# Kernel tuning notes

Hardware: AMD Instinct MI355X
Metric: run time of the kernel (lower is better)

The kernel has to match this reference:

```python
import jax, jax.numpy as jnp
import numpy as np

NUM_ENTITIES = 100000
NUM_TIMES = 10000
D = 512
DB = 768
NUM_REL = 200
NUM_BASES = 4
N_NODES = 30000
N_EDGES = 200000
B = 128
P_ENT = 64
P_TIME = 32
T_UNIQ = 2000


def setup_inputs() -> dict:
    key = jax.random.key(0)
    ks = jax.random.split(key, 32)
    n = jax.random.normal
    ri = jax.random.randint
    inp = {}
    # learned params
    inp['emb'] = n(ks[0], (NUM_ENTITIES + NUM_TIMES, D), jnp.float32) * 0.05
    sc = 1.0 / np.sqrt(D)
    inp['basis1'] = n(ks[1], (NUM_BASES, D, D), jnp.float32) * sc
    inp['att1'] = n(ks[2], (NUM_REL, NUM_BASES), jnp.float32) * 0.5
    inp['root1'] = n(ks[3], (D, D), jnp.float32) * sc
    inp['bias1'] = jnp.zeros((D,), jnp.float32)
    inp['basis2'] = n(ks[4], (NUM_BASES, D, D), jnp.float32) * sc
    inp['att2'] = n(ks[5], (NUM_REL, NUM_BASES), jnp.float32) * 0.5
    inp['root2'] = n(ks[6], (D, D), jnp.float32) * sc
    inp['bias2'] = jnp.zeros((D,), jnp.float32)
    sb = 1.0 / np.sqrt(DB)
    inp['W_lin'] = n(ks[7], (DB, D), jnp.float32) * sb
    inp['b_lin'] = jnp.zeros((D,), jnp.float32)
    inp['W_attn'] = n(ks[8], (DB, D), jnp.float32) * sb
    inp['b_attn'] = jnp.zeros((D,), jnp.float32)
    inp['W_prob'] = n(ks[9], (DB, 1), jnp.float32) * sb
    inp['b_prob'] = jnp.zeros((1,), jnp.float32)
    # forward tensor args
    inp['ques_emb_bert'] = n(ks[10], (B, DB), jnp.float32)
    inp['x_idx'] = ri(ks[11], (N_NODES,), 0, NUM_ENTITIES, jnp.int32)
    inp['edge_index'] = ri(ks[12], (2, N_EDGES), 0, N_NODES, jnp.int32)
    inp['edge_type'] = ri(ks[13], (N_EDGES,), 0, NUM_REL, jnp.int32)
    inp['start_time'] = ri(ks[14], (N_EDGES,), 0, NUM_TIMES, jnp.int32)
    inp['end_time'] = ri(ks[15], (N_EDGES,), 0, NUM_TIMES, jnp.int32)
    inp['edge_batch_idx'] = jnp.sort(ri(ks[16], (N_EDGES,), 0, B, jnp.int32))
    inp['edge_norm'] = jax.random.uniform(ks[17], (N_EDGES,), jnp.float32)
    inp['uniq_times'] = ri(ks[18], (T_UNIQ,), 0, NUM_TIMES, jnp.int32)
    # padded index vectors: positions >= count point at the appended zero row
    ent_counts = ri(ks[19], (B,), 1, P_ENT + 1, jnp.int32)
    time_counts = ri(ks[20], (B,), 1, P_TIME + 1, jnp.int32)
    pe = ri(ks[21], (B, P_ENT), 0, N_NODES, jnp.int32)
    pt = ri(ks[22], (B, P_TIME), 0, T_UNIQ, jnp.int32)
    inp['padded_ent'] = jnp.where(jnp.arange(P_ENT)[None, :] < ent_counts[:, None], pe, N_NODES)
    inp['padded_time'] = jnp.where(jnp.arange(P_TIME)[None, :] < time_counts[:, None], pt, T_UNIQ)
    inp['ent_counts'] = ent_counts
    inp['time_counts'] = time_counts
    return inp


def rgcn_layer(x, basis, att, root, bias, src, dst, etype, st_emb, et_emb, q_t, edge_norm):
    # basis decomposition: project all nodes through each basis once. [N, NB, D]
    xb = jnp.einsum('ni,bio->nbo', x, basis)
    coeff = att[etype]                                 # [E, NB]
    msg = jnp.einsum('eb,ebd->ed', coeff, xb[src])     # [E, D]
    # time gate: question-time embedding vs edge interval midpoint embedding
    gate = jax.nn.sigmoid(jnp.sum(q_t * 0.5 * (st_emb + et_emb), axis=-1))  # [E]
    msg = msg * (gate * edge_norm)[:, None]
    agg = jax.ops.segment_sum(msg, dst, num_segments=N_NODES)
    return agg + x @ root + bias


def reference(emb, basis1, att1, root1, bias1, basis2, att2, root2, bias2,
              W_lin, b_lin, W_attn, b_attn, W_prob, b_prob,
              ques_emb_bert, x_idx, edge_index, edge_type, start_time, end_time,
              edge_batch_idx, edge_norm, uniq_times, padded_ent, padded_time,
              ent_counts, time_counts):
    question_embedding = ques_emb_bert @ W_lin + b_lin                  # [B, D]
    time_for_edge_attn = (ques_emb_bert @ W_attn + b_attn)[edge_batch_idx]  # [E, D]
    st_emb = emb[start_time + NUM_ENTITIES]
    et_emb = emb[end_time + NUM_ENTITIES]
    x = emb[x_idx]                                                      # [N, D]
    src, dst = edge_index[0], edge_index[1]
    h = jax.nn.relu(rgcn_layer(x, basis1, att1, root1, bias1, src, dst, edge_type,
                               st_emb, et_emb, time_for_edge_attn, edge_norm))
    # dropout is identity in eval mode
    h = rgcn_layer(h, basis2, att2, root2, bias2, src, dst, edge_type,
                   st_emb, et_emb, time_for_edge_attn, edge_norm)       # [N, D]
    subgraph_time_emb = emb[uniq_times + NUM_ENTITIES]                  # [T_u, D]
    zero = jnp.zeros((1, D), h.dtype)
    ent_w_zeros = jnp.concatenate([h, zero], axis=0)
    time_w_zeros = jnp.concatenate([subgraph_time_emb, zero], axis=0)
    pooled_ent = jnp.sum(ent_w_zeros[padded_ent], axis=1) / ent_counts[:, None].astype(h.dtype)
    pooled_time = jnp.sum(time_w_zeros[padded_time], axis=1) / time_counts[:, None].astype(h.dtype)
    p_ent = jax.nn.sigmoid(ques_emb_bert @ W_prob + b_prob)             # [B, 1]
    pred = (question_embedding + pooled_ent * p_ent + pooled_time * (1.0 - p_ent)) / 3.0
    # batched cosine similarity against full entity+time vocab
    pred_n = pred / jnp.maximum(jnp.linalg.norm(pred, axis=-1, keepdims=True), 1e-8)
    emb_n = emb / jnp.maximum(jnp.linalg.norm(emb, axis=-1, keepdims=True), 1e-8)
    score = pred_n @ emb_n.T                                            # [B, V]
    return score * 30.0
```

## Files before the change

### kernel.cpp

```cpp
#include <hip/hip_runtime.h>

#define NUM_ENT   100000
#define NTIMES    10000
#define DD        512
#define DB        768
#define NREL      200
#define NBAS      4
#define NN        30000
#define NEDGE     200000
#define BATCH     128
#define PENT      64
#define PTIME     32
#define TUNIQ     2000
#define V_TOT     110000
#define V_PAD     110208
#define VT16      6888
#define M_PAD2    30208
#define MT2R      1888
#define KT_L      80
#define KT_E      16

typedef __attribute__((ext_vector_type(8))) short s8v;
typedef __attribute__((ext_vector_type(4))) float f4v;

__device__ __forceinline__ unsigned short f2bf(float x){
  unsigned int u = __builtin_bit_cast(unsigned int, x);
  u += 0x7fffu + ((u >> 16) & 1u);
  return (unsigned short)(u >> 16);
}
__device__ __forceinline__ float bf2f(unsigned short h){
  unsigned int u = ((unsigned int)h) << 16;
  return __builtin_bit_cast(float, u);
}

__device__ __forceinline__ void gload16(const void* g, void* l){
  __builtin_amdgcn_global_load_lds(
      (const __attribute__((address_space(1))) void*)g,
      (__attribute__((address_space(3))) void*)l, 16, 0, 0);
}


__global__ __launch_bounds__(256) void k_conv_emb(const float* __restrict__ emb,
    unsigned short* __restrict__ Bp, float* __restrict__ invn){
  int vt = blockIdx.x;
  int wid = threadIdx.x >> 6, lane = threadIdx.x & 63;
  int vrow = vt * 16 + (lane & 15);
  float ss = 0.f;
  __shared__ float ssw[4][16];
  for (int i = 0; i < 4; ++i){
    int kt = wid + i * 4;
    int k0 = kt * 32 + (lane >> 4) * 8;
    s8v o;
    if (vrow < V_TOT){
      const float4* p = reinterpret_cast<const float4*>(emb + (size_t)vrow * DD + k0);
      float4 v0 = p[0], v1 = p[1];
      ss += v0.x*v0.x + v0.y*v0.y + v0.z*v0.z + v0.w*v0.w;
      ss += v1.x*v1.x + v1.y*v1.y + v1.z*v1.z + v1.w*v1.w;
      o[0] = (short)f2bf(v0.x); o[1] = (short)f2bf(v0.y);
      o[2] = (short)f2bf(v0.z); o[3] = (short)f2bf(v0.w);
      o[4] = (short)f2bf(v1.x); o[5] = (short)f2bf(v1.y);
      o[6] = (short)f2bf(v1.z); o[7] = (short)f2bf(v1.w);
    } else {
      #pragma unroll
      for (int j = 0; j < 8; ++j) o[j] = 0;
    }
    *reinterpret_cast<s8v*>(Bp + ((size_t)(kt * VT16 + vt) << 9) + lane * 8) = o;
  }
  ss += __shfl_xor(ss, 16);
  ss += __shfl_xor(ss, 32);
  if ((lane >> 4) == 0) ssw[wid][lane] = ss;
  __syncthreads();
  if (threadIdx.x < 16){
    float s = ssw[0][threadIdx.x] + ssw[1][threadIdx.x] + ssw[2][threadIdx.x] + ssw[3][threadIdx.x];
    int v = vt * 16 + threadIdx.x;
    invn[v] = (v < V_TOT) ? (1.0f / fmaxf(sqrtf(s), 1e-8f)) : 0.0f;
  }
}

__global__ __launch_bounds__(256) void k_small2(const float* __restrict__ ques,
    const float* __restrict__ Wl, const float* __restrict__ bl,
    const float* __restrict__ Wa, const float* __restrict__ ba,
    const float* __restrict__ Wp, const float* __restrict__ bp,
    float* __restrict__ qlin, float* __restrict__ qattn, float* __restrict__ pent){
  if (blockIdx.x == 32){
    int b = threadIdx.x >> 1, half = threadIdx.x & 1;
    float a = 0.f;
    int k0 = half * 384;
    for (int k = k0; k < k0 + 384; ++k)
      a = fmaf(ques[(size_t)b * DB + k], Wp[k], a);
    a += __shfl_xor(a, 1);
    if (half == 0) pent[b] = 1.f / (1.f + expf(-(a + bp[0])));
    return;
  }
  __shared__ float sq[128 * 96];
  int col = threadIdx.x & 31, bg = threadIdx.x >> 5;
  int c0 = blockIdx.x * 32;
  const float* W = (c0 < 512) ? Wl : Wa;
  int wcol = (c0 & 511) + col;
  float acc[16] = {};
  for (int k0 = 0; k0 < DB; k0 += 96){
    __syncthreads();
    for (int i = threadIdx.x; i < 128 * 96; i += 256){
      int b = i / 96, kk = i - b * 96;
      sq[i] = ques[(size_t)b * DB + k0 + kk];
    }
    __syncthreads();
    for (int kk = 0; kk < 96; kk += 4){
      float w0 = W[(size_t)(k0 + kk + 0) * 512 + wcol];
      float w1 = W[(size_t)(k0 + kk + 1) * 512 + wcol];
      float w2 = W[(size_t)(k0 + kk + 2) * 512 + wcol];
      float w3 = W[(size_t)(k0 + kk + 3) * 512 + wcol];
      #pragma unroll
      for (int bb = 0; bb < 16; ++bb){
        float4 qv = *reinterpret_cast<const float4*>(&sq[(bg * 16 + bb) * 96 + kk]);
        acc[bb] = fmaf(qv.x, w0, fmaf(qv.y, w1, fmaf(qv.z, w2, fmaf(qv.w, w3, acc[bb]))));
      }
    }
  }
  float* dst = (c0 < 512) ? qlin : qattn;
  const float* bias = (c0 < 512) ? bl : ba;
  #pragma unroll
  for (int bb = 0; bb < 16; ++bb)
    dst[(size_t)(bg * 16 + bb) * 512 + wcol] = acc[bb] + bias[wcol];
}

__global__ __launch_bounds__(256) void k_pack_qrows(const float* __restrict__ src,
    unsigned short* __restrict__ Ap){
  int w = (int)((blockIdx.x * 256 + threadIdx.x) >> 6);
  int lane = threadIdx.x & 63;
  if (w >= BATCH) return;
  const float* p = src + (size_t)w * 512 + lane * 8;
  s8v o;
  #pragma unroll
  for (int j = 0; j < 8; ++j) o[j] = (short)f2bf(p[j]);
  *reinterpret_cast<s8v*>(Ap + ((size_t)((w >> 4) * KT_E + (lane >> 2)) << 9)
                             + ((w & 15) + (lane & 3) * 16) * 8) = o;
}

__global__ __launch_bounds__(256) void k_pack_B(const float* __restrict__ basis,
    const float* __restrict__ root, unsigned short* __restrict__ Bp){
  int idx = blockIdx.x * 256 + threadIdx.x;
  if (idx >= KT_L * 32 * 64) return;
  int lane = idx & 63; int kt = idx >> 11;
  int k0 = kt * 32 + (lane >> 4) * 8;
  int col = ((idx >> 6) & 31) * 16 + (lane & 15);
  s8v o;
  #pragma unroll
  for (int j = 0; j < 8; ++j){
    int k = k0 + j;
    float v = (k < 2048) ? basis[(size_t)k * 512 + col] : root[(size_t)(k - 2048) * 512 + col];
    o[j] = (short)f2bf(v);
  }
  *reinterpret_cast<s8v*>(Bp + (size_t)idx * 8) = o;
}

template<int MODE>
__global__ __launch_bounds__(512, 2) void k_gemm256(
    const unsigned short* __restrict__ A, const unsigned short* __restrict__ B,
    const float* __restrict__ bias, unsigned short* __restrict__ outh){
  __shared__ __align__(1024) short sAll[3 * 16384];
  const int Kt = KT_L;
  int tid = threadIdx.x;
  int lane = tid & 63, wid = tid >> 6;
  int wr = wid >> 2, wc = wid & 3;
  const int q = 29, r = 4;
  int g = blockIdx.x;
  int xcd = g & 7, i = g >> 3;
  int ng = (xcd < r ? xcd * (q + 1) : r * (q + 1) + (xcd - r) * q) + i;
  int blkM = ng >> 1, blkN = ng & 1;
  int rt0 = blkM * 16;
  int ct0 = blkN * 16;
  const unsigned short* pA0 = A + ((size_t)(rt0 + wid) * Kt) * 512 + lane * 8;
  const unsigned short* pA1 = A + ((size_t)(rt0 + 8 + wid) * Kt) * 512 + lane * 8;
  const unsigned short* pB0 = B + (size_t)(ct0 + wid) * 512 + lane * 8;
  const unsigned short* pB1 = B + (size_t)(ct0 + 8 + wid) * 512 + lane * 8;
  const size_t gbs = 32 * 512;
  int soA0 = wid * 512, soA1 = (8 + wid) * 512;
  f4v acc[8][4] = {};

  auto STAGE = [&](int buf, int kt){
    short* b = &sAll[buf * 16384];
    gload16(pA0 + (size_t)kt * 512, b + soA0);
    gload16(pA1 + (size_t)kt * 512, b + soA1);
    gload16(pB0 + (size_t)kt * gbs, b + 8192 + soA0);
    gload16(pB1 + (size_t)kt * gbs, b + 8192 + soA1);
  };
  auto COMPUTE = [&](int buf){
    const short* base = &sAll[buf * 16384];
    s8v af[8], bfr[4];
    #pragma unroll
    for (int m = 0; m < 8; ++m) af[m] = *reinterpret_cast<const s8v*>(base + (wr * 8 + m) * 512 + lane * 8);
    #pragma unroll
    for (int n = 0; n < 4; ++n) bfr[n] = *reinterpret_cast<const s8v*>(base + 8192 + (wc * 4 + n) * 512 + lane * 8);
    __builtin_amdgcn_s_setprio(1);
    #pragma unroll
    for (int m = 0; m < 8; ++m)
      #pragma unroll
      for (int n = 0; n < 4; ++n)
        acc[m][n] = __builtin_amdgcn_mfma_f32_16x16x32_bf16(af[m], bfr[n], acc[m][n], 0, 0, 0);
    __builtin_amdgcn_s_setprio(0);
  };

  STAGE(0, 0);
  STAGE(1, 1);
  int cb = 0, sb = 2;
  for (int kt = 0; kt < Kt - 2; ++kt){
    STAGE(sb, kt + 2);
    asm volatile("s_waitcnt vmcnt(8)" ::: "memory");
    __builtin_amdgcn_s_barrier();
    __builtin_amdgcn_sched_barrier(0);
    COMPUTE(cb);
    __builtin_amdgcn_s_barrier();
    cb = (cb == 2) ? 0 : cb + 1;
    sb = (sb == 2) ? 0 : sb + 1;
  }
  asm volatile("s_waitcnt vmcnt(4)" ::: "memory");
  __builtin_amdgcn_s_barrier();
  __builtin_amdgcn_sched_barrier(0);
  COMPUTE(cb);
  cb = (cb == 2) ? 0 : cb + 1;
  asm volatile("s_waitcnt vmcnt(0)" ::: "memory");
  __builtin_amdgcn_s_barrier();
  __builtin_amdgcn_sched_barrier(0);
  COMPUTE(cb);

  int R0 = blkM * 256 + wr * 128 + (lane >> 4) * 4;
  int C0 = blkN * 256 + wc * 64 + (lane & 15);
  #pragma unroll
  for (int m = 0; m < 8; ++m)
    #pragma unroll
    for (int n = 0; n < 4; ++n){
      int col = C0 + n * 16;
      float bb = bias[col];
      #pragma unroll
      for (int rr4 = 0; rr4 < 4; ++rr4){
        int rr = R0 + m * 16 + rr4;
        if (rr < NN){
          float v = acc[m][n][rr4] + bb;
          if constexpr (MODE == 1) v = fmaxf(v, 0.f);
          outh[(size_t)rr * 512 + col] = f2bf(v);
        }
      }
    }
}

template<int MODE>
__global__ __launch_bounds__(256) void k_gemm(
    const unsigned short* __restrict__ A, const unsigned short* __restrict__ B,
    int Kt, int Bt_stride, int ct_off,
    const float* __restrict__ invn, float* __restrict__ outf){
  __shared__ __align__(1024) short sAll[3 * 8192];
  int tid = threadIdx.x;
  int lane = tid & 63, wid = tid >> 6;
  int wr = wid >> 1, wc = wid & 1;
  int rt0 = blockIdx.x * 8;
  int ct0 = blockIdx.y * 8;
  int ctB = ct0 + ct_off;
  const unsigned short* pA0 = A + ((size_t)(rt0 + 2 * wid) * Kt) * 512 + lane * 8;
  const unsigned short* pA1 = pA0 + (size_t)Kt * 512;
  const unsigned short* pB0 = B + (size_t)(ctB + 2 * wid) * 512 + lane * 8;
  const unsigned short* pB1 = pB0 + 512;
  size_t gbs = (size_t)Bt_stride * 512;
  int so = 2 * wid * 512;
  f4v acc[4][4] = {};

  auto STAGE = [&](int buf, int kt){
    short* b = &sAll[buf * 8192];
    gload16(pA0 + (size_t)kt * 512, b + so);
    gload16(pA1 + (size_t)kt * 512, b + so + 512);
    gload16(pB0 + (size_t)kt * gbs, b + 4096 + so);
    gload16(pB1 + (size_t)kt * gbs, b + 4096 + so + 512);
  };
  auto COMPUTE = [&](int buf){
    const short* base = &sAll[buf * 8192];
    s8v af[4], bfr[4];
    #pragma unroll
    for (int m = 0; m < 4; ++m) af[m] = *reinterpret_cast<const s8v*>(base + (wr * 4 + m) * 512 + lane * 8);
    #pragma unroll
    for (int n = 0; n < 4; ++n) bfr[n] = *reinterpret_cast<const s8v*>(base + 4096 + (wc * 4 + n) * 512 + lane * 8);
    #pragma unroll
    for (int m = 0; m < 4; ++m)
      #pragma unroll
      for (int n = 0; n < 4; ++n)
        acc[m][n] = __builtin_amdgcn_mfma_f32_16x16x32_bf16(af[m], bfr[n], acc[m][n], 0, 0, 0);
  };

  STAGE(0, 0);
  STAGE(1, 1);
  int cb = 0, sb = 2;
  for (int kt = 0; kt < Kt - 2; ++kt){
    STAGE(sb, kt + 2);
    asm volatile("s_waitcnt vmcnt(8)" ::: "memory");
    __builtin_amdgcn_s_barrier();
    __builtin_amdgcn_sched_barrier(0);
    COMPUTE(cb);
    __builtin_amdgcn_s_barrier();
    cb = (cb == 2) ? 0 : cb + 1;
    sb = (sb == 2) ? 0 : sb + 1;
  }
  asm volatile("s_waitcnt vmcnt(4)" ::: "memory");
  __builtin_amdgcn_s_barrier();
  __builtin_amdgcn_sched_barrier(0);
  COMPUTE(cb);
  cb = (cb == 2) ? 0 : cb + 1;
  asm volatile("s_waitcnt vmcnt(0)" ::: "memory");
  __builtin_amdgcn_s_barrier();
  __builtin_amdgcn_sched_barrier(0);
  COMPUTE(cb);

  #pragma unroll
  for (int m = 0; m < 4; ++m)
    #pragma unroll
    for (int n = 0; n < 4; ++n){
      int row0 = rt0 * 16 + (wr * 4 + m) * 16 + ((lane >> 4) * 4);
      int col  = (ct0 + wc * 4 + n) * 16 + (lane & 15);
      #pragma unroll
      for (int r = 0; r < 4; ++r){
        float c = acc[m][n][r];
        int rr = row0 + r;
        if constexpr (MODE == 0){
          if (col < NTIMES) outf[(size_t)rr * NTIMES + col] = c;
        } else {
          if (col < V_TOT) outf[(size_t)rr * V_TOT + col] = c * invn[col] * 30.0f;
        }
      }
    }
}

__global__ __launch_bounds__(256) void k_edge_w(const int* __restrict__ ebatch,
    const int* __restrict__ st, const int* __restrict__ et,
    const float* __restrict__ enorm, const float* __restrict__ M2,
    float* __restrict__ we){
  int e = blockIdx.x * 256 + threadIdx.x;
  if (e >= NEDGE) return;
  int b = ebatch[e];
  float s = 0.5f * (M2[(size_t)b * NTIMES + st[e]] + M2[(size_t)b * NTIMES + et[e]]);
  we[e] = (1.f / (1.f + expf(-s))) * enorm[e];
}

__global__ __launch_bounds__(256) void k_count(const int* __restrict__ ei,
    int* __restrict__ cnt, int* __restrict__ lists){
  int e = blockIdx.x * 256 + threadIdx.x;
  if (e >= NEDGE) return;
  int dst = ei[NEDGE + e];
  int slot = atomicAdd(&cnt[dst], 1);
  if (slot < 64) lists[(size_t)dst * 64 + slot] = e;
}

__global__ __launch_bounds__(256) void k_gather_x(const int* __restrict__ x_idx,
    const unsigned short* __restrict__ Bp, unsigned short* __restrict__ Ap,
    unsigned short* __restrict__ x_rm){
  int w = (int)((blockIdx.x * 256 + threadIdx.x) >> 6);
  int lane = threadIdx.x & 63;
  if (w >= NN) return;
  int v = x_idx[w];
  s8v x = *reinterpret_cast<const s8v*>(
      Bp + ((size_t)(lane >> 2) * VT16 + (v >> 4)) * 512 + ((v & 15) + (lane & 3) * 16) * 8);
  *reinterpret_cast<s8v*>(x_rm + (size_t)w * 512 + lane * 8) = x;
  *reinterpret_cast<s8v*>(Ap + ((size_t)(w >> 4) * KT_L + 64 + (lane >> 2)) * 512
                             + ((w & 15) + (lane & 3) * 16) * 8) = x;
}

__global__ __launch_bounds__(256) void k_pack_rows(const unsigned short* __restrict__ src_rm,
    unsigned short* __restrict__ Ap){
  int w = (int)((blockIdx.x * 256 + threadIdx.x) >> 6);
  int lane = threadIdx.x & 63;
  if (w >= NN) return;
  s8v x = *reinterpret_cast<const s8v*>(src_rm + (size_t)w * 512 + lane * 8);
  *reinterpret_cast<s8v*>(Ap + ((size_t)(w >> 4) * KT_L + 64 + (lane >> 2)) * 512
                             + ((w & 15) + (lane & 3) * 16) * 8) = x;
}

__global__ __launch_bounds__(256) void k_edge_agg(const unsigned short* __restrict__ xsrc,
    const int* __restrict__ ei, const int* __restrict__ etype,
    const float* __restrict__ we, const float* __restrict__ att,
    const int* __restrict__ cnt, const int* __restrict__ lists,
    unsigned short* __restrict__ Ap){
  __shared__ float satt[NREL * NBAS];
  __shared__ int sed[4][64];
  for (int i = threadIdx.x; i < NREL * NBAS; i += 256) satt[i] = att[i];
  int wid = threadIdx.x >> 6, lane = threadIdx.x & 63;
  int n = blockIdx.x * 4 + wid;
  int deg = min(cnt[n], 64);
  int eid = (lane < deg) ? lists[(size_t)n * 64 + lane] : 0x7fffffff;
  int rank = 0;
  for (int j = 0; j < 64; ++j){
    int v = __shfl(eid, j);
    rank += (v < eid) ? 1 : 0;
  }
  __syncthreads();
  if (lane < deg) sed[wid][rank] = eid;
  __syncthreads();
  float acc[NBAS][8] = {};
  if (deg > 0){
    int my_e = sed[wid][(lane < deg) ? lane : 0];
    int my_s = ei[my_e];
    int my_t = etype[my_e];
    float my_w = we[my_e];
    float c0l = my_w * satt[my_t * 4 + 0];
    float c1l = my_w * satt[my_t * 4 + 1];
    float c2l = my_w * satt[my_t * 4 + 2];
    float c3l = my_w * satt[my_t * 4 + 3];
    int s0 = __shfl(my_s, 0);
    s8v xv = *reinterpret_cast<const s8v*>(xsrc + (size_t)s0 * 512 + lane * 8);
    for (int j = 0; j < deg; ++j){
      s8v xn = xv;
      if (j + 1 < deg){
        int sn = __shfl(my_s, j + 1);
        xn = *reinterpret_cast<const s8v*>(xsrc + (size_t)sn * 512 + lane * 8);
      }
      float c0 = __shfl(c0l, j), c1 = __shfl(c1l, j);
      float c2 = __shfl(c2l, j), c3 = __shfl(c3l, j);
      #pragma unroll
      for (int jj = 0; jj < 8; ++jj){
        float x = bf2f((unsigned short)xv[jj]);
        acc[0][jj] = fmaf(c0, x, acc[0][jj]);
        acc[1][jj] = fmaf(c1, x, acc[1][jj]);
        acc[2][jj] = fmaf(c2, x, acc[2][jj]);
        acc[3][jj] = fmaf(c3, x, acc[3][jj]);
      }
      xv = xn;
    }
  }
  #pragma unroll
  for (int b = 0; b < NBAS; ++b){
    s8v o;
    #pragma unroll
    for (int jj = 0; jj < 8; ++jj) o[jj] = (short)f2bf(acc[b][jj]);
    *reinterpret_cast<s8v*>(Ap + ((size_t)(n >> 4) * KT_L + b * 16 + (lane >> 2)) * 512
                               + ((n & 15) + (lane & 3) * 16) * 8) = o;
  }
}

__global__ __launch_bounds__(256) void k_pred(const unsigned short* __restrict__ h2,
    const float* __restrict__ emb, const int* __restrict__ uniq,
    const int* __restrict__ pent_idx, const int* __restrict__ ptime_idx,
    const int* __restrict__ ent_c, const int* __restrict__ time_c,
    const float* __restrict__ qlin, const float* __restrict__ pent,
    unsigned short* __restrict__ Ap_pred){
  int w = (int)((blockIdx.x * 256 + threadIdx.x) >> 6);
  int lane = threadIdx.x & 63;
  if (w >= BATCH) return;
  float ae[8] = {}, at[8] = {};
  for (int j = 0; j < PENT; ++j){
    int idx = pent_idx[w * PENT + j];
    if (idx < NN){
      s8v hv = *reinterpret_cast<const s8v*>(h2 + (size_t)idx * 512 + lane * 8);
      #pragma unroll
      for (int jj = 0; jj < 8; ++jj) ae[jj] += bf2f((unsigned short)hv[jj]);
    }
  }
  for (int j = 0; j < PTIME; ++j){
    int ti = ptime_idx[w * PTIME + j];
    if (ti < TUNIQ){
      const float* p = emb + (size_t)(NUM_ENT + uniq[ti]) * 512 + lane * 8;
      #pragma unroll
      for (int jj = 0; jj < 8; ++jj) at[jj] += p[jj];
    }
  }
  float ce = 1.f / (float)ent_c[w], ct = 1.f / (float)time_c[w];
  float p = pent[w];
  float pr[8]; float ss = 0.f;
  #pragma unroll
  for (int jj = 0; jj < 8; ++jj){
    float v = (qlin[(size_t)w * 512 + lane * 8 + jj] + ae[jj] * ce * p + at[jj] * ct * (1.f - p)) * (1.f / 3.f);
    pr[jj] = v; ss += v * v;
  }
  ss += __shfl_xor(ss, 32); ss += __shfl_xor(ss, 16); ss += __shfl_xor(ss, 8);
  ss += __shfl_xor(ss, 4);  ss += __shfl_xor(ss, 2);  ss += __shfl_xor(ss, 1);
  float inv = 1.f / fmaxf(sqrtf(ss), 1e-8f);
  s8v o;
  #pragma unroll
  for (int jj = 0; jj < 8; ++jj) o[jj] = (short)f2bf(pr[jj] * inv);
  *reinterpret_cast<s8v*>(Ap_pred + ((size_t)((w >> 4) * KT_E + (lane >> 2)) << 9)
                                  + ((w & 15) + (lane & 3) * 16) * 8) = o;
}

extern "C" void kernel_launch(void* const* d_in, const int* in_sizes, int n_in,
                              void* d_out, int out_size, void* d_ws, size_t ws_size,
                              hipStream_t stream){
  const float* emb    = (const float*)d_in[0];
  const float* basis1 = (const float*)d_in[1];
  const float* att1   = (const float*)d_in[2];
  const float* root1  = (const float*)d_in[3];
  const float* bias1  = (const float*)d_in[4];
  const float* basis2 = (const float*)d_in[5];
  const float* att2   = (const float*)d_in[6];
  const float* root2  = (const float*)d_in[7];
  const float* bias2  = (const float*)d_in[8];
  const float* W_lin  = (const float*)d_in[9];
  const float* b_lin  = (const float*)d_in[10];
  const float* W_attn = (const float*)d_in[11];
  const float* b_attn = (const float*)d_in[12];
  const float* W_prob = (const float*)d_in[13];
  const float* b_prob = (const float*)d_in[14];
  const float* ques   = (const float*)d_in[15];
  const int* x_idx    = (const int*)d_in[16];
  const int* eidx     = (const int*)d_in[17];
  const int* etype    = (const int*)d_in[18];
  const int* stime    = (const int*)d_in[19];
  const int* etime    = (const int*)d_in[20];
  const int* ebatch   = (const int*)d_in[21];
  const float* enorm  = (const float*)d_in[22];
  const int* uniq     = (const int*)d_in[23];
  const int* pent_i   = (const int*)d_in[24];
  const int* ptime_i  = (const int*)d_in[25];
  const int* ent_c    = (const int*)d_in[26];
  const int* time_c   = (const int*)d_in[27];
  float* out = (float*)d_out;

  char* w = (char*)d_ws;
  size_t off = 0;
  auto alloc = [&](size_t bytes)->char*{ char* p = w + off; off += (bytes + 255) & ~(size_t)255; return p; };
  unsigned short* Bp_emb = (unsigned short*)alloc((size_t)KT_E * VT16 * 1024);
  float*          invn   = (float*)alloc((size_t)V_PAD * 4);
  unsigned short* Ap     = (unsigned short*)alloc((size_t)MT2R * KT_L * 1024);
  unsigned short* B1p    = (unsigned short*)alloc((size_t)KT_L * 32 * 1024);
  unsigned short* B2p    = (unsigned short*)alloc((size_t)KT_L * 32 * 1024);
  char* xh_base = alloc((size_t)NN * 512 * 2 * 2);
  unsigned short* x_rm = (unsigned short*)xh_base;
  unsigned short* h1   = (unsigned short*)(xh_base + (size_t)NN * 512 * 2);
  unsigned short* h2   = (unsigned short*)xh_base;
  float* M2    = (float*)alloc((size_t)BATCH * NTIMES * 4);
  float* we    = (float*)alloc((size_t)NEDGE * 4);
  float* qlin  = (float*)alloc((size_t)BATCH * 512 * 4);
  float* qattn = (float*)alloc((size_t)BATCH * 512 * 4);
  float* pent  = (float*)alloc(1024);
  unsigned short* Apq    = (unsigned short*)alloc((size_t)8 * KT_E * 1024);
  unsigned short* Appred = (unsigned short*)alloc((size_t)8 * KT_E * 1024);
  int* cnt   = (int*)alloc((size_t)NN * 4);
  int* lists = (int*)alloc((size_t)NN * 64 * 4);
  (void)ws_size; (void)in_sizes; (void)n_in; (void)out_size;

  k_conv_emb<<<VT16, 256, 0, stream>>>(emb, Bp_emb, invn);
  k_small2<<<33, 256, 0, stream>>>(ques, W_lin, b_lin, W_attn, b_attn, W_prob, b_prob,
                                   qlin, qattn, pent);
  k_pack_qrows<<<32, 256, 0, stream>>>(qattn, Apq);
  k_pack_B<<<(KT_L * 32 * 64 + 255) / 256, 256, 0, stream>>>(basis1, root1, B1p);
  k_pack_B<<<(KT_L * 32 * 64 + 255) / 256, 256, 0, stream>>>(basis2, root2, B2p);
  k_gemm<0><<<dim3(1, 79), 256, 0, stream>>>(Apq, Bp_emb, KT_E, VT16, NUM_ENT / 16,
                                             nullptr, M2);
  k_edge_w<<<(NEDGE + 255) / 256, 256, 0, stream>>>(ebatch, stime, etime, enorm, M2, we);
  hipMemsetAsync(cnt, 0, (size_t)NN * 4, stream);
  k_count<<<(NEDGE + 255) / 256, 256, 0, stream>>>(eidx, cnt, lists);
  k_gather_x<<<NN / 4, 256, 0, stream>>>(x_idx, Bp_emb, Ap, x_rm);
  k_edge_agg<<<NN / 4, 256, 0, stream>>>(x_rm, eidx, etype, we, att1, cnt, lists, Ap);
  k_gemm256<1><<<236, 512, 0, stream>>>(Ap, B1p, bias1, h1);
  k_pack_rows<<<NN / 4, 256, 0, stream>>>(h1, Ap);
  k_edge_agg<<<NN / 4, 256, 0, stream>>>(h1, eidx, etype, we, att2, cnt, lists, Ap);
  k_gemm256<2><<<236, 512, 0, stream>>>(Ap, B2p, bias2, h2);
  k_pred<<<32, 256, 0, stream>>>(h2, emb, uniq, pent_i, ptime_i, ent_c, time_c,
                                 qlin, pent, Appred);
  k_gemm<3><<<dim3(1, V_PAD / 128), 256, 0, stream>>>(Appred, Bp_emb, KT_E, VT16, 0,
                                                      invn, out);
}
```

Before: 764.6 us.

## Fuse embedding conversion into score GEMM and retile RGCN GEMMs

Drops the full-vocabulary bf16 pre-conversion pass. The final score kernel now reads fp32 embeddings directly, converts them to bf16 in LDS and computes the column norms on the fly. Only the time-embedding slice is packed for the M2 GEMM, and gather_x converts rows straight from fp32. Edge weighting and destination counting are fused into one kernel, the RGCN GEMMs are retiled to 256x128 tiles with twice as many blocks, and k_pred spreads its work over one block per batch row. The score kernel's register-staged loads with synchronous barriers may hide latency less well than the previous async LDS pipeline.

```diff
diff --git a/kernel.cpp b/kernel.cpp
--- a/kernel.cpp
+++ b/kernel.cpp
@@ -13,12 +13,11 @@
 #define PTIME     32
 #define TUNIQ     2000
 #define V_TOT     110000
-#define V_PAD     110208
-#define VT16      6888
 #define M_PAD2    30208
 #define MT2R      1888
 #define KT_L      80
 #define KT_E      16
+#define TCT       632
 
 typedef __attribute__((ext_vector_type(8))) short s8v;
 typedef __attribute__((ext_vector_type(4))) float f4v;
@@ -39,43 +38,6 @@
       (__attribute__((address_space(3))) void*)l, 16, 0, 0);
 }
 
-
-__global__ __launch_bounds__(256) void k_conv_emb(const float* __restrict__ emb,
-    unsigned short* __restrict__ Bp, float* __restrict__ invn){
-  int vt = blockIdx.x;
-  int wid = threadIdx.x >> 6, lane = threadIdx.x & 63;
-  int vrow = vt * 16 + (lane & 15);
-  float ss = 0.f;
-  __shared__ float ssw[4][16];
-  for (int i = 0; i < 4; ++i){
-    int kt = wid + i * 4;
-    int k0 = kt * 32 + (lane >> 4) * 8;
-    s8v o;
-    if (vrow < V_TOT){
-      const float4* p = reinterpret_cast<const float4*>(emb + (size_t)vrow * DD + k0);
-      float4 v0 = p[0], v1 = p[1];
-      ss += v0.x*v0.x + v0.y*v0.y + v0.z*v0.z + v0.w*v0.w;
-      ss += v1.x*v1.x + v1.y*v1.y + v1.z*v1.z + v1.w*v1.w;
-      o[0] = (short)f2bf(v0.x); o[1] = (short)f2bf(v0.y);
-      o[2] = (short)f2bf(v0.z); o[3] = (short)f2bf(v0.w);
-      o[4] = (short)f2bf(v1.x); o[5] = (short)f2bf(v1.y);
-      o[6] = (short)f2bf(v1.z); o[7] = (short)f2bf(v1.w);
-    } else {
-      #pragma unroll
-      for (int j = 0; j < 8; ++j) o[j] = 0;
-    }
-    *reinterpret_cast<s8v*>(Bp + ((size_t)(kt * VT16 + vt) << 9) + lane * 8) = o;
-  }
-  ss += __shfl_xor(ss, 16);
-  ss += __shfl_xor(ss, 32);
-  if ((lane >> 4) == 0) ssw[wid][lane] = ss;
-  __syncthreads();
-  if (threadIdx.x < 16){
-    float s = ssw[0][threadIdx.x] + ssw[1][threadIdx.x] + ssw[2][threadIdx.x] + ssw[3][threadIdx.x];
-    int v = vt * 16 + threadIdx.x;
-    invn[v] = (v < V_TOT) ? (1.0f / fmaxf(sqrtf(s), 1e-8f)) : 0.0f;
-  }
-}
 
 __global__ __launch_bounds__(256) void k_small2(const float* __restrict__ ques,
     const float* __restrict__ Wl, const float* __restrict__ bl,
@@ -154,51 +116,64 @@
   *reinterpret_cast<s8v*>(Bp + (size_t)idx * 8) = o;
 }
 
-template<int MODE>
-__global__ __launch_bounds__(512, 2) void k_gemm256(
+__global__ __launch_bounds__(256) void k_pack_temb(const float* __restrict__ emb,
+    unsigned short* __restrict__ Bt){
+  int idx = blockIdx.x * 256 + threadIdx.x;
+  if (idx >= KT_E * TCT * 64) return;
+  int lane = idx & 63;
+  int ct = (idx >> 6) % TCT;
+  int kt = idx / (TCT * 64);
+  int c = ct * 16 + (lane & 15);
+  int k0 = kt * 32 + (lane >> 4) * 8;
+  s8v o;
+  if (c < NTIMES){
+    const float* p = emb + (size_t)(NUM_ENT + c) * 512 + k0;
+    #pragma unroll
+    for (int j = 0; j < 8; ++j) o[j] = (short)f2bf(p[j]);
+  } else {
+    #pragma unroll
+    for (int j = 0; j < 8; ++j) o[j] = 0;
+  }
+  *reinterpret_cast<s8v*>(Bt + (size_t)idx * 8) = o;
+}
+
+__global__ __launch_bounds__(256) void k_gemm_m2(
     const unsigned short* __restrict__ A, const unsigned short* __restrict__ B,
-    const float* __restrict__ bias, unsigned short* __restrict__ outh){
-  __shared__ __align__(1024) short sAll[3 * 16384];
-  const int Kt = KT_L;
+    float* __restrict__ outf){
+  __shared__ __align__(1024) short sAll[3 * 8192];
+  const int Kt = KT_E;
   int tid = threadIdx.x;
   int lane = tid & 63, wid = tid >> 6;
-  int wr = wid >> 2, wc = wid & 3;
-  const int q = 29, r = 4;
-  int g = blockIdx.x;
-  int xcd = g & 7, i = g >> 3;
-  int ng = (xcd < r ? xcd * (q + 1) : r * (q + 1) + (xcd - r) * q) + i;
-  int blkM = ng >> 1, blkN = ng & 1;
-  int rt0 = blkM * 16;
-  int ct0 = blkN * 16;
-  const unsigned short* pA0 = A + ((size_t)(rt0 + wid) * Kt) * 512 + lane * 8;
-  const unsigned short* pA1 = A + ((size_t)(rt0 + 8 + wid) * Kt) * 512 + lane * 8;
-  const unsigned short* pB0 = B + (size_t)(ct0 + wid) * 512 + lane * 8;
-  const unsigned short* pB1 = B + (size_t)(ct0 + 8 + wid) * 512 + lane * 8;
-  const size_t gbs = 32 * 512;
-  int soA0 = wid * 512, soA1 = (8 + wid) * 512;
-  f4v acc[8][4] = {};
+  int wr = wid >> 1, wc = wid & 1;
+  int rt0 = blockIdx.x * 8;
+  int ct0 = blockIdx.y * 8;
+  const unsigned short* pA0 = A + ((size_t)(rt0 + 2 * wid) * Kt) * 512 + lane * 8;
+  const unsigned short* pA1 = pA0 + (size_t)Kt * 512;
+  const unsigned short* pB0 = B + (size_t)(ct0 + 2 * wid) * 512 + lane * 8;
+  const unsigned short* pB1 = pB0 + 512;
+  size_t gbs = (size_t)TCT * 512;
+  int so = 2 * wid * 512;
+  f4v acc[4][4] = {};
 
   auto STAGE = [&](int buf, int kt){
-    short* b = &sAll[buf * 16384];
-    gload16(pA0 + (size_t)kt * 512, b + soA0);
-    gload16(pA1 + (size_t)kt * 512, b + soA1);
-    gload16(pB0 + (size_t)kt * gbs, b + 8192 + soA0);
-    gload16(pB1 + (size_t)kt * gbs, b + 8192 + soA1);
+    short* b = &sAll[buf * 8192];
+    gload16(pA0 + (size_t)kt * 512, b + so);
+    gload16(pA1 + (size_t)kt * 512, b + so + 512);
+    gload16(pB0 + (size_t)kt * gbs, b + 4096 + so);
+    gload16(pB1 + (size_t)kt * gbs, b + 4096 + so + 512);
   };
   auto COMPUTE = [&](int buf){
-    const short* base = &sAll[buf * 16384];
-    s8v af[8], bfr[4];
-    #pragma unroll
-    for (int m = 0; m < 8; ++m) af[m] = *reinterpret_cast<const s8v*>(base + (wr * 8 + m) * 512 + lane * 8);
-    #pragma unroll
-    for (int n = 0; n < 4; ++n) bfr[n] = *reinterpret_cast<const s8v*>(base + 8192 + (wc * 4 + n) * 512 + lane * 8);
-    __builtin_amdgcn_s_setprio(1);
-    #pragma unroll
-    for (int m = 0; m < 8; ++m)
+    const short* base = &sAll[buf * 8192];
+    s8v af[4], bfr[4];
+    #pragma unroll
+    for (int m = 0; m < 4; ++m) af[m] = *reinterpret_cast<const s8v*>(base + (wr * 4 + m) * 512 + lane * 8);
+    #pragma unroll
+    for (int n = 0; n < 4; ++n) bfr[n] = *reinterpret_cast<const s8v*>(base + 4096 + (wc * 4 + n) * 512 + lane * 8);
+    #pragma unroll
+    for (int m = 0; m < 4; ++m)
       #pragma unroll
       for (int n = 0; n < 4; ++n)
         acc[m][n] = __builtin_amdgcn_mfma_f32_16x16x32_bf16(af[m], bfr[n], acc[m][n], 0, 0, 0);
-    __builtin_amdgcn_s_setprio(0);
   };
 
   STAGE(0, 0);
@@ -224,65 +199,61 @@
   __builtin_amdgcn_sched_barrier(0);
   COMPUTE(cb);
 
-  int R0 = blkM * 256 + wr * 128 + (lane >> 4) * 4;
-  int C0 = blkN * 256 + wc * 64 + (lane & 15);
-  #pragma unroll
-  for (int m = 0; m < 8; ++m)
+  #pragma unroll
+  for (int m = 0; m < 4; ++m)
     #pragma unroll
     for (int n = 0; n < 4; ++n){
-      int col = C0 + n * 16;
-      float bb = bias[col];
-      #pragma unroll
-      for (int rr4 = 0; rr4 < 4; ++rr4){
-        int rr = R0 + m * 16 + rr4;
-        if (rr < NN){
-          float v = acc[m][n][rr4] + bb;
-          if constexpr (MODE == 1) v = fmaxf(v, 0.f);
-          outh[(size_t)rr * 512 + col] = f2bf(v);
-        }
+      int row0 = rt0 * 16 + (wr * 4 + m) * 16 + ((lane >> 4) * 4);
+      int col  = (ct0 + wc * 4 + n) * 16 + (lane & 15);
+      #pragma unroll
+      for (int r = 0; r < 4; ++r){
+        int rr = row0 + r;
+        if (col < NTIMES) outf[(size_t)rr * NTIMES + col] = acc[m][n][r];
       }
     }
 }
 
 template<int MODE>
-__global__ __launch_bounds__(256) void k_gemm(
+__global__ __launch_bounds__(512, 4) void k_gemm256(
     const unsigned short* __restrict__ A, const unsigned short* __restrict__ B,
-    int Kt, int Bt_stride, int ct_off,
-    const float* __restrict__ invn, float* __restrict__ outf){
-  __shared__ __align__(1024) short sAll[3 * 8192];
+    const float* __restrict__ bias, unsigned short* __restrict__ outh){
+  __shared__ __align__(1024) short sAll[3 * 12288];
+  const int Kt = KT_L;
   int tid = threadIdx.x;
   int lane = tid & 63, wid = tid >> 6;
   int wr = wid >> 1, wc = wid & 1;
-  int rt0 = blockIdx.x * 8;
-  int ct0 = blockIdx.y * 8;
-  int ctB = ct0 + ct_off;
-  const unsigned short* pA0 = A + ((size_t)(rt0 + 2 * wid) * Kt) * 512 + lane * 8;
-  const unsigned short* pA1 = pA0 + (size_t)Kt * 512;
-  const unsigned short* pB0 = B + (size_t)(ctB + 2 * wid) * 512 + lane * 8;
-  const unsigned short* pB1 = pB0 + 512;
-  size_t gbs = (size_t)Bt_stride * 512;
-  int so = 2 * wid * 512;
+  int g = blockIdx.x;
+  int ng = (g & 7) * 59 + (g >> 3);
+  int blkM = ng >> 2, blkN = ng & 3;
+  int rt0 = blkM * 16;
+  int ct0 = blkN * 8;
+  const unsigned short* pA0 = A + ((size_t)(rt0 + wid) * Kt) * 512 + lane * 8;
+  const unsigned short* pA1 = A + ((size_t)(rt0 + 8 + wid) * Kt) * 512 + lane * 8;
+  const unsigned short* pB0 = B + (size_t)(ct0 + wid) * 512 + lane * 8;
+  const size_t gbs = 32 * 512;
+  int soA0 = wid * 512, soA1 = (8 + wid) * 512, soB = 8192 + wid * 512;
   f4v acc[4][4] = {};
 
   auto STAGE = [&](int buf, int kt){
-    short* b = &sAll[buf * 8192];
-    gload16(pA0 + (size_t)kt * 512, b + so);
-    gload16(pA1 + (size_t)kt * 512, b + so + 512);
-    gload16(pB0 + (size_t)kt * gbs, b + 4096 + so);
-    gload16(pB1 + (size_t)kt * gbs, b + 4096 + so + 512);
+    short* b = &sAll[buf * 12288];
+    gload16(pA0 + (size_t)kt * 512, b + soA0);
+    gload16(pA1 + (size_t)kt * 512, b + soA1);
+    gload16(pB0 + (size_t)kt * gbs, b + soB);
   };
   auto COMPUTE = [&](int buf){
-    const short* base = &sAll[buf * 8192];
+    const short* base = &sAll[buf * 12288];
     s8v af[4], bfr[4];
     #pragma unroll
     for (int m = 0; m < 4; ++m) af[m] = *reinterpret_cast<const s8v*>(base + (wr * 4 + m) * 512 + lane * 8);
     #pragma unroll
-    for (int n = 0; n < 4; ++n) bfr[n] = *reinterpret_cast<const s8v*>(base + 4096 + (wc * 4 + n) * 512 + lane * 8);
+    for (int n = 0; n < 4; ++n) bfr[n] = *reinterpret_cast<const s8v*>(base + 8192 + (wc * 4 + n) * 512 + lane * 8);
+    __builtin_amdgcn_s_setprio(1);
     #pragma unroll
     for (int m = 0; m < 4; ++m)
       #pragma unroll
       for (int n = 0; n < 4; ++n)
         acc[m][n] = __builtin_amdgcn_mfma_f32_16x16x32_bf16(af[m], bfr[n], acc[m][n], 0, 0, 0);
+    __builtin_amdgcn_s_setprio(0);
   };
 
   STAGE(0, 0);
@@ -290,7 +261,7 @@
   int cb = 0, sb = 2;
   for (int kt = 0; kt < Kt - 2; ++kt){
     STAGE(sb, kt + 2);
-    asm volatile("s_waitcnt vmcnt(8)" ::: "memory");
+    asm volatile("s_waitcnt vmcnt(6)" ::: "memory");
     __builtin_amdgcn_s_barrier();
     __builtin_amdgcn_sched_barrier(0);
     COMPUTE(cb);
@@ -298,7 +269,7 @@
     cb = (cb == 2) ? 0 : cb + 1;
     sb = (sb == 2) ? 0 : sb + 1;
   }
-  asm volatile("s_waitcnt vmcnt(4)" ::: "memory");
+  asm volatile("s_waitcnt vmcnt(3)" ::: "memory");
   __builtin_amdgcn_s_barrier();
   __builtin_amdgcn_sched_barrier(0);
   COMPUTE(cb);
@@ -308,54 +279,53 @@
   __builtin_amdgcn_sched_barrier(0);
   COMPUTE(cb);
 
+  int R0 = blkM * 256 + wr * 64 + (lane >> 4) * 4;
+  int C0 = blkN * 128 + wc * 64 + (lane & 15);
   #pragma unroll
   for (int m = 0; m < 4; ++m)
     #pragma unroll
     for (int n = 0; n < 4; ++n){
-      int row0 = rt0 * 16 + (wr * 4 + m) * 16 + ((lane >> 4) * 4);
-      int col  = (ct0 + wc * 4 + n) * 16 + (lane & 15);
-      #pragma unroll
-      for (int r = 0; r < 4; ++r){
-        float c = acc[m][n][r];
-        int rr = row0 + r;
-        if constexpr (MODE == 0){
-          if (col < NTIMES) outf[(size_t)rr * NTIMES + col] = c;
-        } else {
-          if (col < V_TOT) outf[(size_t)rr * V_TOT + col] = c * invn[col] * 30.0f;
+      int col = C0 + n * 16;
+      float bb = bias[col];
+      #pragma unroll
+      for (int r4 = 0; r4 < 4; ++r4){
+        int rr = R0 + m * 16 + r4;
+        if (rr < NN){
+          float v = acc[m][n][r4] + bb;
+          if constexpr (MODE == 1) v = fmaxf(v, 0.f);
+          outh[(size_t)rr * 512 + col] = f2bf(v);
         }
       }
     }
 }
 
-__global__ __launch_bounds__(256) void k_edge_w(const int* __restrict__ ebatch,
+__global__ __launch_bounds__(256) void k_edgeprep(const int* __restrict__ ebatch,
     const int* __restrict__ st, const int* __restrict__ et,
     const float* __restrict__ enorm, const float* __restrict__ M2,
-    float* __restrict__ we){
+    const int* __restrict__ ei,
+    float* __restrict__ we, int* __restrict__ cnt, int* __restrict__ lists){
   int e = blockIdx.x * 256 + threadIdx.x;
   if (e >= NEDGE) return;
   int b = ebatch[e];
   float s = 0.5f * (M2[(size_t)b * NTIMES + st[e]] + M2[(size_t)b * NTIMES + et[e]]);
   we[e] = (1.f / (1.f + expf(-s))) * enorm[e];
-}
-
-__global__ __launch_bounds__(256) void k_count(const int* __restrict__ ei,
-    int* __restrict__ cnt, int* __restrict__ lists){
-  int e = blockIdx.x * 256 + threadIdx.x;
-  if (e >= NEDGE) return;
   int dst = ei[NEDGE + e];
   int slot = atomicAdd(&cnt[dst], 1);
   if (slot < 64) lists[(size_t)dst * 64 + slot] = e;
 }
 
 __global__ __launch_bounds__(256) void k_gather_x(const int* __restrict__ x_idx,
-    const unsigned short* __restrict__ Bp, unsigned short* __restrict__ Ap,
+    const float* __restrict__ emb, unsigned short* __restrict__ Ap,
     unsigned short* __restrict__ x_rm){
   int w = (int)((blockIdx.x * 256 + threadIdx.x) >> 6);
   int lane = threadIdx.x & 63;
   if (w >= NN) return;
   int v = x_idx[w];
-  s8v x = *reinterpret_cast<const s8v*>(
-      Bp + ((size_t)(lane >> 2) * VT16 + (v >> 4)) * 512 + ((v & 15) + (lane & 3) * 16) * 8);
+  const float4* p = reinterpret_cast<const float4*>(emb + (size_t)v * 512 + lane * 8);
+  float4 a = p[0], b = p[1];
+  s8v x;
+  x[0] = (short)f2bf(a.x); x[1] = (short)f2bf(a.y); x[2] = (short)f2bf(a.z); x[3] = (short)f2bf(a.w);
+  x[4] = (short)f2bf(b.x); x[5] = (short)f2bf(b.y); x[6] = (short)f2bf(b.z); x[7] = (short)f2bf(b.w);
   *reinterpret_cast<s8v*>(x_rm + (size_t)w * 512 + lane * 8) = x;
   *reinterpret_cast<s8v*>(Ap + ((size_t)(w >> 4) * KT_L + 64 + (lane >> 2)) * 512
                              + ((w & 15) + (lane & 3) * 16) * 8) = x;
@@ -438,42 +408,148 @@
     const int* __restrict__ ent_c, const int* __restrict__ time_c,
     const float* __restrict__ qlin, const float* __restrict__ pent,
     unsigned short* __restrict__ Ap_pred){
-  int w = (int)((blockIdx.x * 256 + threadIdx.x) >> 6);
-  int lane = threadIdx.x & 63;
-  if (w >= BATCH) return;
-  float ae[8] = {}, at[8] = {};
-  for (int j = 0; j < PENT; ++j){
-    int idx = pent_idx[w * PENT + j];
-    if (idx < NN){
-      s8v hv = *reinterpret_cast<const s8v*>(h2 + (size_t)idx * 512 + lane * 8);
-      #pragma unroll
-      for (int jj = 0; jj < 8; ++jj) ae[jj] += bf2f((unsigned short)hv[jj]);
-    }
-  }
-  for (int j = 0; j < PTIME; ++j){
-    int ti = ptime_idx[w * PTIME + j];
-    if (ti < TUNIQ){
-      const float* p = emb + (size_t)(NUM_ENT + uniq[ti]) * 512 + lane * 8;
-      #pragma unroll
-      for (int jj = 0; jj < 8; ++jj) at[jj] += p[jj];
-    }
-  }
-  float ce = 1.f / (float)ent_c[w], ct = 1.f / (float)time_c[w];
-  float p = pent[w];
-  float pr[8]; float ss = 0.f;
-  #pragma unroll
-  for (int jj = 0; jj < 8; ++jj){
-    float v = (qlin[(size_t)w * 512 + lane * 8 + jj] + ae[jj] * ce * p + at[jj] * ct * (1.f - p)) * (1.f / 3.f);
-    pr[jj] = v; ss += v * v;
-  }
-  ss += __shfl_xor(ss, 32); ss += __shfl_xor(ss, 16); ss += __shfl_xor(ss, 8);
-  ss += __shfl_xor(ss, 4);  ss += __shfl_xor(ss, 2);  ss += __shfl_xor(ss, 1);
-  float inv = 1.f / fmaxf(sqrtf(ss), 1e-8f);
-  s8v o;
-  #pragma unroll
-  for (int jj = 0; jj < 8; ++jj) o[jj] = (short)f2bf(pr[jj] * inv);
-  *reinterpret_cast<s8v*>(Ap_pred + ((size_t)((w >> 4) * KT_E + (lane >> 2)) << 9)
-                                  + ((w & 15) + (lane & 3) * 16) * 8) = o;
+  __shared__ float sacc[4][512];
+  int b = blockIdx.x;
+  int wid = threadIdx.x >> 6, lane = threadIdx.x & 63;
+  float a[8] = {};
+  if (wid < 2){
+    for (int j = wid * 32; j < wid * 32 + 32; ++j){
+      int idx = pent_idx[b * PENT + j];
+      if (idx < NN){
+        s8v hv = *reinterpret_cast<const s8v*>(h2 + (size_t)idx * 512 + lane * 8);
+        #pragma unroll
+        for (int jj = 0; jj < 8; ++jj) a[jj] += bf2f((unsigned short)hv[jj]);
+      }
+    }
+  } else {
+    for (int j = (wid - 2) * 16; j < (wid - 2) * 16 + 16; ++j){
+      int ti = ptime_idx[b * PTIME + j];
+      if (ti < TUNIQ){
+        const float* p = emb + (size_t)(NUM_ENT + uniq[ti]) * 512 + lane * 8;
+        #pragma unroll
+        for (int jj = 0; jj < 8; ++jj) a[jj] += p[jj];
+      }
+    }
+  }
+  #pragma unroll
+  for (int jj = 0; jj < 8; ++jj) sacc[wid][lane * 8 + jj] = a[jj];
+  __syncthreads();
+  if (wid == 0){
+    float ce = 1.f / (float)ent_c[b], ct = 1.f / (float)time_c[b];
+    float p = pent[b];
+    float pr[8]; float ss = 0.f;
+    #pragma unroll
+    for (int jj = 0; jj < 8; ++jj){
+      int i = lane * 8 + jj;
+      float ae = sacc[0][i] + sacc[1][i];
+      float at = sacc[2][i] + sacc[3][i];
+      float v = (qlin[(size_t)b * 512 + i] + ae * ce * p + at * ct * (1.f - p)) * (1.f / 3.f);
+      pr[jj] = v; ss += v * v;
+    }
+    ss += __shfl_xor(ss, 32); ss += __shfl_xor(ss, 16); ss += __shfl_xor(ss, 8);
+    ss += __shfl_xor(ss, 4);  ss += __shfl_xor(ss, 2);  ss += __shfl_xor(ss, 1);
+    float inv = 1.f / fmaxf(sqrtf(ss), 1e-8f);
+    s8v o;
+    #pragma unroll
+    for (int jj = 0; jj < 8; ++jj) o[jj] = (short)f2bf(pr[jj] * inv);
+    *reinterpret_cast<s8v*>(Ap_pred + ((size_t)((b >> 4) * KT_E + (lane >> 2)) << 9)
+                                    + ((b & 15) + (lane & 3) * 16) * 8) = o;
+  }
+}
+
+__global__ __launch_bounds__(512) void k_score(
+    const unsigned short* __restrict__ Apred, const float* __restrict__ emb,
+    float* __restrict__ out){
+  __shared__ __align__(1024) short sA[2][4096];
+  __shared__ __align__(1024) short sB[2][8192];
+  __shared__ float sf[512];
+  int tid = threadIdx.x;
+  int lane = tid & 63, wid = tid >> 6;
+  int wr = wid >> 2, wc = wid & 3;
+  int c0 = blockIdx.x * 256;
+  int bc = tid & 255;
+  int kh = tid >> 8;
+  int col_l = bc;
+  int colg = c0 + col_l;
+  bool cval = colg < V_TOT;
+  const float* gB = emb + (size_t)colg * 512 + kh * 16;
+  int ctl = bc >> 4;
+  int wb0 = ctl * 512 + ((2 * kh + 0) * 16 + (bc & 15)) * 8;
+  int wb1 = wb0 + 128;
+  const unsigned short* gA = Apred + ((size_t)wid * KT_E) * 512 + lane * 8;
+  float ss = 0.f;
+  float4 q0, q1, q2, q3;
+  f4v acc[4][4] = {};
+
+  auto LOADB = [&](int s){
+    if (cval){
+      const float4* p = reinterpret_cast<const float4*>(gB + s * 32);
+      q0 = p[0]; q1 = p[1]; q2 = p[2]; q3 = p[3];
+    } else {
+      q0 = q1 = q2 = q3 = float4{0.f, 0.f, 0.f, 0.f};
+    }
+  };
+  auto WRITEB = [&](int p){
+    short* bb = &sB[p][0];
+    s8v o0, o1;
+    o0[0] = (short)f2bf(q0.x); o0[1] = (short)f2bf(q0.y); o0[2] = (short)f2bf(q0.z); o0[3] = (short)f2bf(q0.w);
+    o0[4] = (short)f2bf(q1.x); o0[5] = (short)f2bf(q1.y); o0[6] = (short)f2bf(q1.z); o0[7] = (short)f2bf(q1.w);
+    o1[0] = (short)f2bf(q2.x); o1[1] = (short)f2bf(q2.y); o1[2] = (short)f2bf(q2.z); o1[3] = (short)f2bf(q2.w);
+    o1[4] = (short)f2bf(q3.x); o1[5] = (short)f2bf(q3.y); o1[6] = (short)f2bf(q3.z); o1[7] = (short)f2bf(q3.w);
+    ss += q0.x*q0.x + q0.y*q0.y + q0.z*q0.z + q0.w*q0.w;
+    ss += q1.x*q1.x + q1.y*q1.y + q1.z*q1.z + q1.w*q1.w;
+    ss += q2.x*q2.x + q2.y*q2.y + q2.z*q2.z + q2.w*q2.w;
+    ss += q3.x*q3.x + q3.y*q3.y + q3.z*q3.z + q3.w*q3.w;
+    *reinterpret_cast<s8v*>(bb + wb0) = o0;
+    *reinterpret_cast<s8v*>(bb + wb1) = o1;
+  };
+  auto COMPUTE = [&](int p){
+    s8v af[4], bfr[4];
+    #pragma unroll
+    for (int m = 0; m < 4; ++m) af[m] = *reinterpret_cast<const s8v*>(&sA[p][(wr * 4 + m) * 512 + lane * 8]);
+    #pragma unroll
+    for (int n = 0; n < 4; ++n) bfr[n] = *reinterpret_cast<const s8v*>(&sB[p][(wc * 4 + n) * 512 + lane * 8]);
+    #pragma unroll
+    for (int m = 0; m < 4; ++m)
+      #pragma unroll
+      for (int n = 0; n < 4; ++n)
+        acc[m][n] = __builtin_amdgcn_mfma_f32_16x16x32_bf16(af[m], bfr[n], acc[m][n], 0, 0, 0);
+  };
+
+  LOADB(0);
+  gload16(gA, &sA[0][wid * 512]);
+  for (int s = 0; s < 16; ++s){
+    int p = s & 1;
+    WRITEB(p);
+    __syncthreads();
+    if (s < 15){
+      LOADB(s + 1);
+      gload16(gA + (size_t)(s + 1) * 512, &sA[p ^ 1][wid * 512]);
+    }
+    COMPUTE(p);
+    __syncthreads();
+  }
+  sf[tid] = ss;
+  __syncthreads();
+
+  int R0 = wr * 64 + (lane >> 4) * 4;
+  int C0l = wc * 64 + (lane & 15);
+  #pragma unroll
+  for (int n = 0; n < 4; ++n){
+    int cl = C0l + n * 16;
+    int col = c0 + cl;
+    float s2 = sf[cl] + sf[cl + 256];
+    float inv = (1.f / fmaxf(sqrtf(s2), 1e-8f)) * 30.0f;
+    if (col < V_TOT){
+      #pragma unroll
+      for (int m = 0; m < 4; ++m)
+        #pragma unroll
+        for (int r4 = 0; r4 < 4; ++r4){
+          int rr = R0 + m * 16 + r4;
+          out[(size_t)rr * V_TOT + col] = acc[m][n][r4] * inv;
+        }
+    }
+  }
 }
 
 extern "C" void kernel_launch(void* const* d_in, const int* in_sizes, int n_in,
@@ -512,11 +588,10 @@
   char* w = (char*)d_ws;
   size_t off = 0;
   auto alloc = [&](size_t bytes)->char*{ char* p = w + off; off += (bytes + 255) & ~(size_t)255; return p; };
-  unsigned short* Bp_emb = (unsigned short*)alloc((size_t)KT_E * VT16 * 1024);
-  float*          invn   = (float*)alloc((size_t)V_PAD * 4);
-  unsigned short* Ap     = (unsigned short*)alloc((size_t)MT2R * KT_L * 1024);
-  unsigned short* B1p    = (unsigned short*)alloc((size_t)KT_L * 32 * 1024);
-  unsigned short* B2p    = (unsigned short*)alloc((size_t)KT_L * 32 * 1024);
+  unsigned short* Ap   = (unsigned short*)alloc((size_t)MT2R * KT_L * 1024);
+  unsigned short* B1p  = (unsigned short*)alloc((size_t)KT_L * 32 * 1024);
+  unsigned short* B2p  = (unsigned short*)alloc((size_t)KT_L * 32 * 1024);
+  unsigned short* Bt   = (unsigned short*)alloc((size_t)KT_E * TCT * 1024);
   char* xh_base = alloc((size_t)NN * 512 * 2 * 2);
   unsigned short* x_rm = (unsigned short*)xh_base;
   unsigned short* h1   = (unsigned short*)(xh_base + (size_t)NN * 512 * 2);
@@ -532,25 +607,23 @@
   int* lists = (int*)alloc((size_t)NN * 64 * 4);
   (void)ws_size; (void)in_sizes; (void)n_in; (void)out_size;
 
-  k_conv_emb<<<VT16, 256, 0, stream>>>(emb, Bp_emb, invn);
   k_small2<<<33, 256, 0, stream>>>(ques, W_lin, b_lin, W_attn, b_attn, W_prob, b_prob,
                                    qlin, qattn, pent);
   k_pack_qrows<<<32, 256, 0, stream>>>(qattn, Apq);
   k_pack_B<<<(KT_L * 32 * 64 + 255) / 256, 256, 0, stream>>>(basis1, root1, B1p);
   k_pack_B<<<(KT_L * 32 * 64 + 255) / 256, 256, 0, stream>>>(basis2, root2, B2p);
-  k_gemm<0><<<dim3(1, 79), 256, 0, stream>>>(Apq, Bp_emb, KT_E, VT16, NUM_ENT / 16,
-                                             nullptr, M2);
-  k_edge_w<<<(NEDGE + 255) / 256, 256, 0, stream>>>(ebatch, stime, etime, enorm, M2, we);
+  k_pack_temb<<<(KT_E * TCT * 64) / 256, 256, 0, stream>>>(emb, Bt);
+  k_gemm_m2<<<dim3(1, 79), 256, 0, stream>>>(Apq, Bt, M2);
   hipMemsetAsync(cnt, 0, (size_t)NN * 4, stream);
-  k_count<<<(NEDGE + 255) / 256, 256, 0, stream>>>(eidx, cnt, lists);
-  k_gather_x<<<NN / 4, 256, 0, stream>>>(x_idx, Bp_emb, Ap, x_rm);
+  k_edgeprep<<<(NEDGE + 255) / 256, 256, 0, stream>>>(ebatch, stime, etime, enorm, M2,
+                                                      eidx, we, cnt, lists);
+  k_gather_x<<<NN / 4, 256, 0, stream>>>(x_idx, emb, Ap, x_rm);
   k_edge_agg<<<NN / 4, 256, 0, stream>>>(x_rm, eidx, etype, we, att1, cnt, lists, Ap);
-  k_gemm256<1><<<236, 512, 0, stream>>>(Ap, B1p, bias1, h1);
+  k_gemm256<1><<<472, 512, 0, stream>>>(Ap, B1p, bias1, h1);
   k_pack_rows<<<NN / 4, 256, 0, stream>>>(h1, Ap);
   k_edge_agg<<<NN / 4, 256, 0, stream>>>(h1, eidx, etype, we, att2, cnt, lists, Ap);
-  k_gemm256<2><<<236, 512, 0, stream>>>(Ap, B2p, bias2, h2);
-  k_pred<<<32, 256, 0, stream>>>(h2, emb, uniq, pent_i, ptime_i, ent_c, time_c,
-                                 qlin, pent, Appred);
-  k_gemm<3><<<dim3(1, V_PAD / 128), 256, 0, stream>>>(Appred, Bp_emb, KT_E, VT16, 0,
-                                                      invn, out);
-}
+  k_gemm256<2><<<472, 512, 0, stream>>>(Ap, B2p, bias2, h2);
+  k_pred<<<BATCH, 256, 0, stream>>>(h2, emb, uniq, pent_i, ptime_i, ent_c, time_c,
+                                    qlin, pent, Appred);
+  k_score<<<430, 512, 0, stream>>>(Appred, emb, out);
+}
```

New measurement: 719.3 us. 5.9% less time.
